# Kernel tuning notes

Hardware: AMD Instinct MI355X
Metric: run time of the kernel (lower is better)

## Reference

```python
import jax, jax.numpy as jnp
import numpy as np

B, T, C = 4, 2048, 1024
HEADS = 16
HEAD_DIM = C // HEADS
WINDOW = 256


def setup_inputs() -> dict:
    key = jax.random.key(0)
    k1, k2, k3 = jax.random.split(key, 3)
    x = jax.random.normal(k1, (B, T, C), dtype=jnp.float32)
    # torch nn.Linear weights: [out_features, in_features]; scale like kaiming-uniform-ish
    W_qkv = jax.random.normal(k2, (3 * C, C), dtype=jnp.float32) * (1.0 / np.sqrt(C))
    W_proj = jax.random.normal(k3, (C, C), dtype=jnp.float32) * (1.0 / np.sqrt(C))
    return {"x": x, "W_qkv": W_qkv, "W_proj": W_proj}


def reference(x, W_qkv, W_proj):
    b, t, c = x.shape
    h, d = HEADS, HEAD_DIM
    qkv = x @ W_qkv.T  # [b,t,3c]
    q, k, v = jnp.split(qkv, 3, axis=-1)
    q = q.reshape(b, t, h, d).transpose(0, 2, 1, 3)  # [b,h,t,d]
    k = k.reshape(b, t, h, d).transpose(0, 2, 1, 3)
    v = v.reshape(b, t, h, d).transpose(0, 2, 1, 3)
    scale = 1.0 / jnp.sqrt(jnp.asarray(d, dtype=q.dtype))
    scores = jnp.einsum('bhqd,bhkd->bhqk', q, k) * scale  # [b,h,t,t]
    i = jnp.arange(t)[:, None]
    j = jnp.arange(t)[None, :]
    mask = (j <= i) & (j > i - WINDOW)  # sliding-window causal band
    scores = jnp.where(mask, scores, -jnp.inf)
    attn = jax.nn.softmax(scores, axis=-1)
    y = jnp.einsum('bhqk,bhkd->bhqd', attn, v)  # [b,h,t,d]
    y = y.transpose(0, 2, 1, 3).reshape(b, t, c)
    return y @ W_proj.T
```

## Files before the change

### kernel.cpp

```cpp
#include <hip/hip_runtime.h>
#include <hip/hip_bf16.h>
#include <math.h>

#define BB 4
#define TT 2048
#define CC 1024
#define HH 16
#define DD 64
#define WW 256
#define MM (BB*TT)
#define NX (MM*CC)
#define NQ (3*CC*CC)
#define NP (CC*CC)

typedef __bf16 bf16x8 __attribute__((ext_vector_type(8)));
typedef __bf16 bf16x4 __attribute__((ext_vector_type(4)));
typedef float  f32x4  __attribute__((ext_vector_type(4)));

__device__ __forceinline__ void async_cp16(const void* g, void* l) {
  __builtin_amdgcn_global_load_lds(
      (const __attribute__((address_space(1))) void*)g,
      (__attribute__((address_space(3))) void*)l, 16, 0, 0);
}

__device__ __forceinline__ unsigned short f2bf(float v) {
  __hip_bfloat16 h = __float2bfloat16(v);
  return *(unsigned short*)&h;
}

__global__ __launch_bounds__(256)
void prep(const float* __restrict__ x,
          const float* __restrict__ wq,
          const float* __restrict__ wp,
          __hip_bfloat16* __restrict__ wdst,
          unsigned short* __restrict__ Apk) {
  const int p = blockIdx.x;
  const int tid = threadIdx.x;
  if (p < 4096) {
    int i = (p * 256 + tid) * 4;
    const float* src; int off;
    if (i < NQ) { src = wq; off = i; }
    else        { src = wp; off = i - NQ; }
    float4 v = *(const float4*)(src + off);
    wdst[i + 0] = __float2bfloat16(v.x);
    wdst[i + 1] = __float2bfloat16(v.y);
    wdst[i + 2] = __float2bfloat16(v.z);
    wdst[i + 3] = __float2bfloat16(v.w);
    return;
  }
  __shared__ __align__(16) unsigned short tile[64 * 72];
  const int pid = p - 4096;
  const int bm = pid & 127;
  const int bk = pid >> 7;
  const int tr = tid >> 4;
  const int tc = (tid & 15) * 4;
#pragma unroll
  for (int i = 0; i < 4; i++) {
    int row = i * 16 + tr;
    float4 v = *(const float4*)&x[(size_t)(bm * 64 + row) * 1024 + bk * 64 + tc];
    tile[row * 72 + tc + 0] = f2bf(v.x);
    tile[row * 72 + tc + 1] = f2bf(v.y);
    tile[row * 72 + tc + 2] = f2bf(v.z);
    tile[row * 72 + tc + 3] = f2bf(v.w);
  }
  __syncthreads();
  const int w = tid >> 6, lane = tid & 63;
  const int quad = lane >> 4, l15 = lane & 15;
#pragma unroll
  for (int f = 0; f < 2; f++) {
    bf16x8 fr = *(const bf16x8*)&tile[(w * 16 + l15) * 72 + f * 32 + quad * 8];
    *(bf16x8*)&Apk[(((size_t)(bm * 4 + w) * 32) + bk * 2 + f) * 512 + lane * 8] = fr;
  }
}

__global__ __launch_bounds__(256, 2)
void gemm_qkv(const unsigned short* __restrict__ Apk,
              const unsigned short* __restrict__ Bw,
              unsigned short* __restrict__ Qh,
              unsigned short* __restrict__ Kh,
              unsigned short* __restrict__ Vt) {
  __shared__ __align__(16) unsigned short Bs[4][8192];

  const int id   = blockIdx.x;
  const int xcd  = id & 7;
  const int slot = id >> 3;
  const int mloc = slot / 24;
  const int nloc = slot % 24;
  const int m0 = (xcd * 4 + mloc) * 256;
  const int n0 = nloc * 128;

  const int tid  = threadIdx.x;
  const int w    = tid >> 6;
  const int lane = tid & 63;
  const int quad = lane >> 4;
  const int l15  = lane & 15;

  f32x4 acc[4][8];
#pragma unroll
  for (int i = 0; i < 4; i++)
#pragma unroll
    for (int j = 0; j < 8; j++) acc[i][j] = (f32x4)0.0f;

  const unsigned short* abase =
      Apk + ((size_t)((m0 >> 4) + w * 4) * 32) * 512 + lane * 8;

  auto stageB = [&](int k0, unsigned short* bs) {
#pragma unroll
    for (int i = 0; i < 4; i++) {
      int idx  = w + 4 * i;
      int kc   = idx >> 1;
      int half = idx & 1;
      async_cp16(Bw + (size_t)(n0 + half * 64 + lane) * 1024 + k0 + kc * 8,
                 &bs[kc * 1024 + half * 512]);
    }
  };

  bf16x8 Af[3][4];
  auto loadA = [&](int g, bf16x8* fr) {
#pragma unroll
    for (int tm = 0; tm < 4; tm++)
      fr[tm] = *(const bf16x8*)(abase + ((size_t)(tm * 32 + g)) * 512);
  };

  loadA(0, Af[0]);
  loadA(1, Af[1]);
  stageB(0,   Bs[0]);
  stageB(64,  Bs[1]);
  stageB(128, Bs[2]);
  asm volatile("s_waitcnt vmcnt(0)" ::: "memory");
  __builtin_amdgcn_sched_barrier(0);
  asm volatile("s_barrier" ::: "memory");

#pragma unroll
  for (int s = 0; s < 16; s++) {
    const unsigned short* bs = Bs[s & 3];
    if (s + 3 < 16) stageB((s + 3) * 64, Bs[(s + 3) & 3]);
#pragma unroll
    for (int sub = 0; sub < 2; sub++) {
      const int g = s * 2 + sub;
      if (g + 2 < 32) loadA(g + 2, Af[(g + 2) % 3]);
      const bf16x8* af = Af[g % 3];
      __builtin_amdgcn_s_setprio(1);
#pragma unroll
      for (int tn = 0; tn < 8; tn++) {
        bf16x8 bfv = *(const bf16x8*)
            &bs[(sub * 4 + quad) * 1024 + (tn * 16 + l15) * 8];
#pragma unroll
        for (int tm = 0; tm < 4; tm++)
          acc[tm][tn] = __builtin_amdgcn_mfma_f32_16x16x32_bf16(
              af[tm], bfv, acc[tm][tn], 0, 0, 0);
      }
      __builtin_amdgcn_s_setprio(0);
    }
    asm volatile("s_waitcnt vmcnt(16) lgkmcnt(0)" ::: "memory");
    __builtin_amdgcn_sched_barrier(0);
    asm volatile("s_barrier" ::: "memory");
  }

  const int t3 = n0 >> 10;
  if (t3 < 2) {
    unsigned short* dst0 = (t3 == 0) ? Qh : Kh;
    const float sc = (t3 == 0) ? 0.125f : 1.0f;
#pragma unroll
    for (int tm = 0; tm < 4; tm++)
#pragma unroll
      for (int tn = 0; tn < 8; tn++) {
        int colb = n0 + tn * 16;
        int hh = (colb >> 6) & 15;
        int dd = (colb & 63) + l15;
#pragma unroll
        for (int r = 0; r < 4; r++) {
          int row = m0 + w * 64 + tm * 16 + quad * 4 + r;
          int b = row >> 11, tt = row & 2047;
          dst0[((size_t)((b * 16 + hh) * 2048 + tt)) * 64 + dd] =
              f2bf(acc[tm][tn][r] * sc);
        }
      }
  } else {
    unsigned short* T = &Bs[0][0] + w * 4608;
    const int b    = (m0 + w * 64) >> 11;
    const int tc_g = ((m0 & 2047) >> 6) + w;
    const int h0   = (n0 >> 6) & 15;
#pragma unroll
    for (int hp = 0; hp < 2; hp++) {
#pragma unroll
      for (int tnl = 0; tnl < 4; tnl++)
#pragma unroll
        for (int tm = 0; tm < 4; tm++)
#pragma unroll
          for (int r = 0; r < 4; r++)
            T[(tnl * 16 + l15) * 72 + tm * 16 + quad * 4 + r] =
                f2bf(acc[tm][hp * 4 + tnl][r]);
      asm volatile("s_waitcnt lgkmcnt(0)" ::: "memory");
      const size_t base =
          ((size_t)((b * 16 + h0 + hp) * 32 + tc_g)) * 4096;
#pragma unroll
      for (int i = 0; i < 8; i++) {
        int d   = i * 8 + (lane >> 3);
        int tin = (lane & 7) * 8;
        bf16x8 v = *(const bf16x8*)&T[d * 72 + tin];
        *(bf16x8*)&Vt[base + (size_t)d * 64 + tin] = v;
      }
    }
  }
}

__global__ __launch_bounds__(256, 2)
void gemm_proj(const unsigned short* __restrict__ Apk,
               const unsigned short* __restrict__ Bw,
               float* __restrict__ Co) {
  __shared__ __align__(16) unsigned short Bs[4][8192];

  const int id   = blockIdx.x;
  const int xcd  = id & 7;
  const int slot = id >> 3;
  const int mloc = slot >> 3;
  const int nloc = slot & 7;
  const int m0 = (xcd * 8 + mloc) * 128;
  const int n0 = nloc * 128;

  const int tid  = threadIdx.x;
  const int w    = tid >> 6;
  const int lane = tid & 63;
  const int quad = lane >> 4;
  const int l15  = lane & 15;

  f32x4 acc[2][8];
#pragma unroll
  for (int i = 0; i < 2; i++)
#pragma unroll
    for (int j = 0; j < 8; j++) acc[i][j] = (f32x4)0.0f;

  const unsigned short* abase =
      Apk + ((size_t)((m0 >> 4) + w * 2) * 32) * 512 + lane * 8;

  auto stageB = [&](int k0, unsigned short* bs) {
#pragma unroll
    for (int i = 0; i < 4; i++) {
      int idx  = w + 4 * i;
      int kc   = idx >> 1;
      int half = idx & 1;
      async_cp16(Bw + (size_t)(n0 + half * 64 + lane) * 1024 + k0 + kc * 8,
                 &bs[kc * 1024 + half * 512]);
    }
  };

  bf16x8 Af[3][2];
  auto loadA = [&](int g, bf16x8* fr) {
#pragma unroll
    for (int tm = 0; tm < 2; tm++)
      fr[tm] = *(const bf16x8*)(abase + ((size_t)(tm * 32 + g)) * 512);
  };

  loadA(0, Af[0]);
  loadA(1, Af[1]);
  stageB(0,   Bs[0]);
  stageB(64,  Bs[1]);
  stageB(128, Bs[2]);
  asm volatile("s_waitcnt vmcnt(0)" ::: "memory");
  __builtin_amdgcn_sched_barrier(0);
  asm volatile("s_barrier" ::: "memory");

#pragma unroll
  for (int s = 0; s < 16; s++) {
    const unsigned short* bs = Bs[s & 3];
    if (s + 3 < 16) stageB((s + 3) * 64, Bs[(s + 3) & 3]);
#pragma unroll
    for (int sub = 0; sub < 2; sub++) {
      const int g = s * 2 + sub;
      if (g + 2 < 32) loadA(g + 2, Af[(g + 2) % 3]);
      const bf16x8* af = Af[g % 3];
      __builtin_amdgcn_s_setprio(1);
#pragma unroll
      for (int tn = 0; tn < 8; tn++) {
        bf16x8 bfv = *(const bf16x8*)
            &bs[(sub * 4 + quad) * 1024 + (tn * 16 + l15) * 8];
#pragma unroll
        for (int tm = 0; tm < 2; tm++)
          acc[tm][tn] = __builtin_amdgcn_mfma_f32_16x16x32_bf16(
              af[tm], bfv, acc[tm][tn], 0, 0, 0);
      }
      __builtin_amdgcn_s_setprio(0);
    }
    if (s < 14)
      asm volatile("s_waitcnt vmcnt(12) lgkmcnt(0)" ::: "memory");
    else
      asm volatile("s_waitcnt vmcnt(8) lgkmcnt(0)" ::: "memory");
    __builtin_amdgcn_sched_barrier(0);
    asm volatile("s_barrier" ::: "memory");
  }

#pragma unroll
  for (int tm = 0; tm < 2; tm++)
#pragma unroll
    for (int tn = 0; tn < 8; tn++)
#pragma unroll
      for (int r = 0; r < 4; r++) {
        int row = m0 + w * 32 + tm * 16 + quad * 4 + r;
        int col = n0 + tn * 16 + l15;
        Co[(size_t)row * 1024 + col] = acc[tm][tn][r];
      }
}

__global__ __launch_bounds__(256, 2)
void attn_mfma(const unsigned short* __restrict__ Qh,
               const unsigned short* __restrict__ Kh,
               const unsigned short* __restrict__ Vt,
               unsigned short* __restrict__ Ypk) {
  __shared__ __align__(16) unsigned short SH[40960];

  const int tid  = threadIdx.x;
  const int w    = tid >> 6;
  const int lane = tid & 63;
  const int quad = lane >> 4;
  const int l15  = lane & 15;
  const int q0 = blockIdx.x * 64;
  const int bh = blockIdx.y;

  const int c0 = (q0 >= 256) ? 0 : (4 - (q0 >> 6));

  const unsigned short* Qg = Qh + ((size_t)bh * 2048 + q0) * 64;
  bf16x8 Qf[2];
#pragma unroll
  for (int fs = 0; fs < 2; fs++)
    Qf[fs] = *(const bf16x8*)(Qg + (w * 16 + l15) * 64 + fs * 32 + quad * 8);

  const unsigned short* Kg = Kh + (size_t)bh * 2048 * 64;
  const unsigned short* Vg = Vt + (size_t)bh * 32 * 4096;
  for (int ch = c0; ch < 5; ch++) {
    int sc = q0 - 256 + ch * 64;
#pragma unroll
    for (int i = 0; i < 2; i++) {
      int kc = w * 2 + i;
      async_cp16(Kg + (size_t)(sc + lane) * 64 + kc * 8,
                 &SH[ch * 4096 + kc * 512]);
      async_cp16(Vg + (size_t)(sc >> 6) * 4096 + lane * 64 + kc * 8,
                 &SH[20480 + ch * 4096 + kc * 512]);
    }
  }
  __syncthreads();

  f32x4 S[5][4];
#pragma unroll
  for (int ch = 0; ch < 5; ch++)
#pragma unroll
    for (int tn = 0; tn < 4; tn++) S[ch][tn] = (f32x4)0.0f;

#pragma unroll
  for (int ch = 0; ch < 5; ch++) {
    if (ch < c0) continue;
#pragma unroll
    for (int ks = 0; ks < 2; ks++) {
      int kc = ks * 4 + quad;
#pragma unroll
      for (int tn = 0; tn < 4; tn++) {
        bf16x8 bk = *(const bf16x8*)
            &SH[ch * 4096 + kc * 512 + (tn * 16 + l15) * 8];
        S[ch][tn] = __builtin_amdgcn_mfma_f32_16x16x32_bf16(
            Qf[ks], bk, S[ch][tn], 0, 0, 0);
      }
    }
  }

  const int qb = q0 + w * 16 + quad * 4;
  if (c0 == 0) {
#pragma unroll
    for (int tn = 0; tn < 4; tn++) {
      int j = q0 - 256 + tn * 16 + l15;
#pragma unroll
      for (int r = 0; r < 4; r++)
        if (qb + r > j + (WW - 1)) S[0][tn][r] = -__builtin_inff();
    }
  }
#pragma unroll
  for (int tn = 0; tn < 4; tn++) {
    int j = q0 + tn * 16 + l15;
#pragma unroll
    for (int r = 0; r < 4; r++)
      if (j > qb + r) S[4][tn][r] = -__builtin_inff();
  }

  float mrow[4], lrow[4];
#pragma unroll
  for (int r = 0; r < 4; r++) mrow[r] = -__builtin_inff();
#pragma unroll
  for (int ch = 0; ch < 5; ch++) {
    if (ch < c0) continue;
#pragma unroll
    for (int tn = 0; tn < 4; tn++)
#pragma unroll
      for (int r = 0; r < 4; r++)
        mrow[r] = fmaxf(mrow[r], S[ch][tn][r]);
  }
#pragma unroll
  for (int off = 1; off < 16; off <<= 1)
#pragma unroll
    for (int r = 0; r < 4; r++)
      mrow[r] = fmaxf(mrow[r], __shfl_xor(mrow[r], off));

#pragma unroll
  for (int r = 0; r < 4; r++) lrow[r] = 0.0f;
#pragma unroll
  for (int ch = 0; ch < 5; ch++) {
    if (ch < c0) continue;
#pragma unroll
    for (int tn = 0; tn < 4; tn++)
#pragma unroll
      for (int r = 0; r < 4; r++) {
        float e = __expf(S[ch][tn][r] - mrow[r]);
        S[ch][tn][r] = e;
        lrow[r] += e;
      }
  }
#pragma unroll
  for (int off = 1; off < 16; off <<= 1)
#pragma unroll
    for (int r = 0; r < 4; r++) lrow[r] += __shfl_xor(lrow[r], off);

  __syncthreads();

  f32x4 Oacc[4];
#pragma unroll
  for (int td = 0; td < 4; td++) Oacc[td] = (f32x4)0.0f;

#pragma unroll
  for (int ch = 0; ch < 5; ch++) {
    if (ch < c0) continue;
    unsigned short* Ps = SH + (ch & 1) * 4608;
#pragma unroll
    for (int tn = 0; tn < 4; tn++)
#pragma unroll
      for (int r = 0; r < 4; r++)
        Ps[(w * 16 + quad * 4 + r) * 68 + tn * 16 + l15] = f2bf(S[ch][tn][r]);
    asm volatile("s_waitcnt lgkmcnt(0)" ::: "memory");
#pragma unroll
    for (int ks = 0; ks < 2; ks++) {
      int off = (w * 16 + l15) * 68 + ks * 32 + quad * 8;
      bf16x4 plo = *(const bf16x4*)&Ps[off];
      bf16x4 phi = *(const bf16x4*)&Ps[off + 4];
      bf16x8 ap = __builtin_shufflevector(plo, phi, 0, 1, 2, 3, 4, 5, 6, 7);
      int kc = ks * 4 + quad;
#pragma unroll
      for (int td = 0; td < 4; td++) {
        bf16x8 bv = *(const bf16x8*)
            &SH[20480 + ch * 4096 + kc * 512 + (td * 16 + l15) * 8];
        Oacc[td] = __builtin_amdgcn_mfma_f32_16x16x32_bf16(
            ap, bv, Oacc[td], 0, 0, 0);
      }
    }
  }

  const int b = bh >> 4, h = bh & 15;
  float inv[4];
#pragma unroll
  for (int r = 0; r < 4; r++) inv[r] = 1.0f / lrow[r];
  unsigned short* Ot = SH + 10240;
#pragma unroll
  for (int td = 0; td < 4; td++)
#pragma unroll
    for (int r = 0; r < 4; r++)
      Ot[(w * 16 + quad * 4 + r) * 72 + td * 16 + l15] =
          f2bf(Oacc[td][r] * inv[r]);
  asm volatile("s_waitcnt lgkmcnt(0)" ::: "memory");
  const size_t rt = (size_t)((b * 2048 + q0) >> 4) + w;
#pragma unroll
  for (int f = 0; f < 2; f++) {
    bf16x8 fr = *(const bf16x8*)&Ot[(w * 16 + l15) * 72 + f * 32 + quad * 8];
    *(bf16x8*)&Ypk[(rt * 32 + h * 2 + f) * 512 + lane * 8] = fr;
  }
}

extern "C" void kernel_launch(void* const* d_in, const int* in_sizes, int n_in,
                              void* d_out, int out_size, void* d_ws, size_t ws_size,
                              hipStream_t stream) {
  const float* x     = (const float*)d_in[0];
  const float* wqkv  = (const float*)d_in[1];
  const float* wproj = (const float*)d_in[2];
  float* out = (float*)d_out;

  char* ws = (char*)d_ws;
  unsigned short* apk    = (unsigned short*)(ws);
  unsigned short* wqkvb  = (unsigned short*)(ws + (size_t)16 * 1024 * 1024);
  unsigned short* wprojb = (unsigned short*)(ws + (size_t)22 * 1024 * 1024);
  unsigned short* qh     = (unsigned short*)(ws + (size_t)24 * 1024 * 1024);
  unsigned short* kh     = (unsigned short*)(ws + (size_t)40 * 1024 * 1024);
  unsigned short* vt     = (unsigned short*)(ws + (size_t)56 * 1024 * 1024);
  unsigned short* ypk    = (unsigned short*)(ws + (size_t)72 * 1024 * 1024);

  prep<<<4096 + 2048, 256, 0, stream>>>(
      x, wqkv, wproj, (__hip_bfloat16*)wqkvb, apk);

  gemm_qkv<<<768, 256, 0, stream>>>(apk, wqkvb, qh, kh, vt);

  attn_mfma<<<dim3(TT / 64, BB * HH), 256, 0, stream>>>(
      qh, kh, vt, ypk);

  gemm_proj<<<512, 256, 0, stream>>>(ypk, wprojb, out);
}
```

Measured before the change: 219.2 us.

## Pre-pack weights and K/V into tile-contiguous layouts for coalesced async copies

The prep kernel now writes bf16 weights in a blocked layout where each 64x8 sub-tile is 512 contiguous elements, so the GEMM B-stage loads read fully contiguous 1KB chunks instead of strided rows. The QKV epilogue writes K (and V) in the same chunked tile layout, so the attention kernel's K/V staging also becomes contiguous per-wave loads. The intent is better global-memory coalescing for the async-to-LDS copies. In exchange the prep weight scatter writes become scattered 2-byte stores, and the K epilogue store pattern changes.

After: 212.9 us. 2.9% less time.

```diff
diff --git a/kernel.cpp b/kernel.cpp
--- a/kernel.cpp
+++ b/kernel.cpp
@@ -28,24 +28,34 @@
   return *(unsigned short*)&h;
 }
 
+__device__ __forceinline__ size_t wpk_off(int n, int k) {
+  return ((((size_t)(n >> 7) * 16 + (k >> 6)) * 16) +
+          (((k >> 3) & 7) * 2 + ((n >> 6) & 1))) * 512 +
+         (size_t)(n & 63) * 8 + (k & 7);
+}
+
 __global__ __launch_bounds__(256)
 void prep(const float* __restrict__ x,
           const float* __restrict__ wq,
           const float* __restrict__ wp,
-          __hip_bfloat16* __restrict__ wdst,
+          unsigned short* __restrict__ wpk,
           unsigned short* __restrict__ Apk) {
   const int p = blockIdx.x;
   const int tid = threadIdx.x;
   if (p < 4096) {
     int i = (p * 256 + tid) * 4;
-    const float* src; int off;
-    if (i < NQ) { src = wq; off = i; }
-    else        { src = wp; off = i - NQ; }
-    float4 v = *(const float4*)(src + off);
-    wdst[i + 0] = __float2bfloat16(v.x);
-    wdst[i + 1] = __float2bfloat16(v.y);
-    wdst[i + 2] = __float2bfloat16(v.z);
-    wdst[i + 3] = __float2bfloat16(v.w);
+    const float* src; unsigned short* dst; int n, k;
+    if (i < NQ) { src = wq + i; n = i >> 10; k = i & 1023; dst = wpk; }
+    else {
+      int j = i - NQ;
+      src = wp + j; n = j >> 10; k = j & 1023; dst = wpk + NQ;
+    }
+    float4 v = *(const float4*)src;
+    size_t off = wpk_off(n, k);
+    dst[off + 0] = f2bf(v.x);
+    dst[off + 1] = f2bf(v.y);
+    dst[off + 2] = f2bf(v.z);
+    dst[off + 3] = f2bf(v.w);
     return;
   }
   __shared__ __align__(16) unsigned short tile[64 * 72];
@@ -104,14 +114,14 @@
   const unsigned short* abase =
       Apk + ((size_t)((m0 >> 4) + w * 4) * 32) * 512 + lane * 8;
 
-  auto stageB = [&](int k0, unsigned short* bs) {
+  const unsigned short* wb = Bw + (size_t)(n0 >> 7) * (16 * 16 * 512);
+
+  auto stageB = [&](int kt, unsigned short* bs) {
 #pragma unroll
     for (int i = 0; i < 4; i++) {
-      int idx  = w + 4 * i;
-      int kc   = idx >> 1;
-      int half = idx & 1;
-      async_cp16(Bw + (size_t)(n0 + half * 64 + lane) * 1024 + k0 + kc * 8,
-                 &bs[kc * 1024 + half * 512]);
+      int idx = w + 4 * i;
+      async_cp16(wb + ((size_t)kt * 16 + idx) * 512 + lane * 8,
+                 &bs[idx * 512]);
     }
   };
 
@@ -124,9 +134,9 @@
 
   loadA(0, Af[0]);
   loadA(1, Af[1]);
-  stageB(0,   Bs[0]);
-  stageB(64,  Bs[1]);
-  stageB(128, Bs[2]);
+  stageB(0, Bs[0]);
+  stageB(1, Bs[1]);
+  stageB(2, Bs[2]);
   asm volatile("s_waitcnt vmcnt(0)" ::: "memory");
   __builtin_amdgcn_sched_barrier(0);
   asm volatile("s_barrier" ::: "memory");
@@ -134,7 +144,7 @@
 #pragma unroll
   for (int s = 0; s < 16; s++) {
     const unsigned short* bs = Bs[s & 3];
-    if (s + 3 < 16) stageB((s + 3) * 64, Bs[(s + 3) & 3]);
+    if (s + 3 < 16) stageB(s + 3, Bs[(s + 3) & 3]);
 #pragma unroll
     for (int sub = 0; sub < 2; sub++) {
       const int g = s * 2 + sub;
@@ -158,9 +168,7 @@
   }
 
   const int t3 = n0 >> 10;
-  if (t3 < 2) {
-    unsigned short* dst0 = (t3 == 0) ? Qh : Kh;
-    const float sc = (t3 == 0) ? 0.125f : 1.0f;
+  if (t3 == 0) {
 #pragma unroll
     for (int tm = 0; tm < 4; tm++)
 #pragma unroll
@@ -172,8 +180,24 @@
         for (int r = 0; r < 4; r++) {
           int row = m0 + w * 64 + tm * 16 + quad * 4 + r;
           int b = row >> 11, tt = row & 2047;
-          dst0[((size_t)((b * 16 + hh) * 2048 + tt)) * 64 + dd] =
-              f2bf(acc[tm][tn][r] * sc);
+          Qh[((size_t)((b * 16 + hh) * 2048 + tt)) * 64 + dd] =
+              f2bf(acc[tm][tn][r] * 0.125f);
+        }
+      }
+  } else if (t3 == 1) {
+#pragma unroll
+    for (int tm = 0; tm < 4; tm++)
+#pragma unroll
+      for (int tn = 0; tn < 8; tn++) {
+        int colb = n0 + tn * 16;
+        int hh = (colb >> 6) & 15;
+        int dd = (colb & 63) + l15;
+#pragma unroll
+        for (int r = 0; r < 4; r++) {
+          int row = m0 + w * 64 + tm * 16 + quad * 4 + r;
+          int b = row >> 11, tt = row & 2047;
+          Kh[((((size_t)(b * 16 + hh) * 32 + (tt >> 6)) * 8 + (dd >> 3)) * 512)
+             + (tt & 63) * 8 + (dd & 7)] = f2bf(acc[tm][tn][r]);
         }
       }
   } else {
@@ -195,11 +219,9 @@
       const size_t base =
           ((size_t)((b * 16 + h0 + hp) * 32 + tc_g)) * 4096;
 #pragma unroll
-      for (int i = 0; i < 8; i++) {
-        int d   = i * 8 + (lane >> 3);
-        int tin = (lane & 7) * 8;
-        bf16x8 v = *(const bf16x8*)&T[d * 72 + tin];
-        *(bf16x8*)&Vt[base + (size_t)d * 64 + tin] = v;
+      for (int j = 0; j < 8; j++) {
+        bf16x8 v = *(const bf16x8*)&T[lane * 72 + j * 8];
+        *(bf16x8*)&Vt[base + (size_t)j * 512 + lane * 8] = v;
       }
     }
   }
@@ -234,14 +256,14 @@
   const unsigned short* abase =
       Apk + ((size_t)((m0 >> 4) + w * 2) * 32) * 512 + lane * 8;
 
-  auto stageB = [&](int k0, unsigned short* bs) {
+  const unsigned short* wb = Bw + (size_t)(n0 >> 7) * (16 * 16 * 512);
+
+  auto stageB = [&](int kt, unsigned short* bs) {
 #pragma unroll
     for (int i = 0; i < 4; i++) {
-      int idx  = w + 4 * i;
-      int kc   = idx >> 1;
-      int half = idx & 1;
-      async_cp16(Bw + (size_t)(n0 + half * 64 + lane) * 1024 + k0 + kc * 8,
-                 &bs[kc * 1024 + half * 512]);
+      int idx = w + 4 * i;
+      async_cp16(wb + ((size_t)kt * 16 + idx) * 512 + lane * 8,
+                 &bs[idx * 512]);
     }
   };
 
@@ -254,9 +276,9 @@
 
   loadA(0, Af[0]);
   loadA(1, Af[1]);
-  stageB(0,   Bs[0]);
-  stageB(64,  Bs[1]);
-  stageB(128, Bs[2]);
+  stageB(0, Bs[0]);
+  stageB(1, Bs[1]);
+  stageB(2, Bs[2]);
   asm volatile("s_waitcnt vmcnt(0)" ::: "memory");
   __builtin_amdgcn_sched_barrier(0);
   asm volatile("s_barrier" ::: "memory");
@@ -264,7 +286,7 @@
 #pragma unroll
   for (int s = 0; s < 16; s++) {
     const unsigned short* bs = Bs[s & 3];
-    if (s + 3 < 16) stageB((s + 3) * 64, Bs[(s + 3) & 3]);
+    if (s + 3 < 16) stageB(s + 3, Bs[(s + 3) & 3]);
 #pragma unroll
     for (int sub = 0; sub < 2; sub++) {
       const int g = s * 2 + sub;
@@ -325,16 +347,16 @@
   for (int fs = 0; fs < 2; fs++)
     Qf[fs] = *(const bf16x8*)(Qg + (w * 16 + l15) * 64 + fs * 32 + quad * 8);
 
-  const unsigned short* Kg = Kh + (size_t)bh * 2048 * 64;
+  const unsigned short* Kg = Kh + (size_t)bh * 32 * 4096;
   const unsigned short* Vg = Vt + (size_t)bh * 32 * 4096;
   for (int ch = c0; ch < 5; ch++) {
-    int sc = q0 - 256 + ch * 64;
+    int tc = (q0 >> 6) - 4 + ch;
 #pragma unroll
     for (int i = 0; i < 2; i++) {
       int kc = w * 2 + i;
-      async_cp16(Kg + (size_t)(sc + lane) * 64 + kc * 8,
+      async_cp16(Kg + ((size_t)tc * 8 + kc) * 512 + lane * 8,
                  &SH[ch * 4096 + kc * 512]);
-      async_cp16(Vg + (size_t)(sc >> 6) * 4096 + lane * 64 + kc * 8,
+      async_cp16(Vg + ((size_t)tc * 8 + kc) * 512 + lane * 8,
                  &SH[20480 + ch * 4096 + kc * 512]);
     }
   }
@@ -487,8 +509,7 @@
   unsigned short* vt     = (unsigned short*)(ws + (size_t)56 * 1024 * 1024);
   unsigned short* ypk    = (unsigned short*)(ws + (size_t)72 * 1024 * 1024);
 
-  prep<<<4096 + 2048, 256, 0, stream>>>(
-      x, wqkv, wproj, (__hip_bfloat16*)wqkvb, apk);
+  prep<<<4096 + 2048, 256, 0, stream>>>(x, wqkv, wproj, wqkvb, apk);
 
   gemm_qkv<<<768, 256, 0, stream>>>(apk, wqkvb, qh, kh, vt);
 
```
